# Kernel optimization log

Hardware: AMD Instinct MI355X
Metric: run time of the kernel (lower is better)

Reference implementation:

```python
import jax, jax.numpy as jnp
import numpy as np

N, E, D, H, C = 50000, 800000, 64, 2, 64  # nodes, edges, feat, heads, per-head out


def _transformer_conv(x, src, dst, wq, bq, wk, bk, wv, bv, ws, bs):
    n = x.shape[0]
    q = (x @ wq + bq).reshape(n, H, C)
    k = (x @ wk + bk).reshape(n, H, C)
    v = (x @ wv + bv).reshape(n, H, C)
    qi = q[dst]           # [E,H,C] gather at target nodes
    kj = k[src]           # [E,H,C] gather at source nodes
    vj = v[src]
    alpha = jnp.einsum('ehc,ehc->eh', qi, kj) / jnp.sqrt(jnp.asarray(C, x.dtype))
    # segment softmax over incoming edges of each dst node
    amax = jax.ops.segment_max(alpha, dst, num_segments=n)          # [N,H]
    amax = jnp.where(jnp.isfinite(amax), amax, 0.0)
    ex = jnp.exp(alpha - amax[dst])                                  # [E,H]
    denom = jax.ops.segment_sum(ex, dst, num_segments=n)            # [N,H]
    a = ex / (denom[dst] + 1e-16)
    out = jax.ops.segment_sum(a[:, :, None] * vj, dst, num_segments=n)  # [N,H,C]
    out = out.mean(axis=1)                                           # concat=False -> mean heads
    return out + x @ ws + bs                                         # root (skip) connection


def setup_inputs() -> dict:
    key = jax.random.key(0)
    ks = jax.random.split(key, 20)
    x = jax.random.normal(ks[0], (N, D), dtype=jnp.float32)
    edge_index = jax.random.randint(ks[1], (2, E), 0, N, dtype=jnp.int64)
    s = 1.0 / np.sqrt(D)
    def lin(k, din, dout):
        return jax.random.uniform(k, (din, dout), jnp.float32, -s, s)
    inp = {"x": x, "edge_index": edge_index}
    i = 2
    for l, din in ((1, D), (2, C)):
        for nm, dout in (("wq", H * C), ("wk", H * C), ("wv", H * C), ("ws", C)):
            inp[f"l{l}_{nm}"] = lin(ks[i], din, dout); i += 1
            inp[f"l{l}_{nm.replace('w','b')}"] = jnp.zeros((dout,), jnp.float32)
    return inp


def reference(x, edge_index,
              l1_wq, l1_bq, l1_wk, l1_bk, l1_wv, l1_bv, l1_ws, l1_bs,
              l2_wq, l2_bq, l2_wk, l2_bk, l2_wv, l2_bv, l2_ws, l2_bs):
    src, dst = edge_index[0], edge_index[1]
    h = _transformer_conv(x, src, dst, l1_wq, l1_bq, l1_wk, l1_bk, l1_wv, l1_bv, l1_ws, l1_bs)
    h = _transformer_conv(h, src, dst, l2_wq, l2_bq, l2_wk, l2_bk, l2_wv, l2_bv, l2_ws, l2_bs)
    return h
```

## Files before the change

### kernel.cpp

```cpp
#include <hip/hip_runtime.h>
#include <hip/hip_fp16.h>
#include <math.h>


typedef _Float16 half8 __attribute__((ext_vector_type(8)));
typedef _Float16 half4 __attribute__((ext_vector_type(4)));
typedef float floatx4 __attribute__((ext_vector_type(4)));

struct __align__(16) H8 { __half2 a, b, c, d; };
struct __align__(16) F16x8 { _Float16 v[8]; };

static __device__ inline __half2 shfl_xor_h2(__half2 v, int off) {
    union { __half2 h; int i; } u;
    u.h = v;
    u.i = __shfl_xor(u.i, off);
    return u.h;
}

__global__ __launch_bounds__(256) void prep_w_both(
    const float* __restrict__ W0, const float* __restrict__ B0,
    const float* __restrict__ W1, const float* __restrict__ B1,
    const float* __restrict__ W2, const float* __restrict__ B2,
    const float* __restrict__ W3, const float* __restrict__ B3,
    const float* __restrict__ W4, const float* __restrict__ B4,
    const float* __restrict__ W5, const float* __restrict__ B5,
    const float* __restrict__ W6, const float* __restrict__ B6,
    const float* __restrict__ W7, const float* __restrict__ B7,
    _Float16* __restrict__ wht1, _Float16* __restrict__ wht2,
    float* __restrict__ ball1, float* __restrict__ ball2,
    int* __restrict__ counts, int n) {
    const int tid = blockIdx.x * 256 + threadIdx.x;
    const int nt  = gridDim.x * 256;
    for (int idx = tid; idx < 448 * 64; idx += nt) {
        int c = idx >> 6, k = idx & 63;
        float v1, v2;
        if (c < 128)      { v1 = W0[k*128 + c];       v2 = W4[k*128 + c]; }
        else if (c < 256) { v1 = W1[k*128 + (c-128)]; v2 = W5[k*128 + (c-128)]; }
        else if (c < 384) { v1 = W2[k*128 + (c-256)]; v2 = W6[k*128 + (c-256)]; }
        else              { v1 = W3[k*64 + (c-384)];  v2 = W7[k*64 + (c-384)]; }
        wht1[c*64 + k] = (_Float16)v1;
        wht2[c*64 + k] = (_Float16)v2;
        if (k == 0) {
            float b1, b2;
            if (c < 128)      { b1 = B0[c];     b2 = B4[c]; }
            else if (c < 256) { b1 = B1[c-128]; b2 = B5[c-128]; }
            else if (c < 384) { b1 = B2[c-256]; b2 = B6[c-256]; }
            else              { b1 = B3[c-384]; b2 = B7[c-384]; }
            ball1[c] = b1;
            ball2[c] = b2;
        }
    }
    for (int i = tid; i < n; i += nt) counts[i] = 0;
}

template <int F32IN>
static __device__ __forceinline__ void gemm_tile_body(
    const void* __restrict__ Xin, int rows,
    const _Float16* __restrict__ WhT, const float* __restrict__ Ball,
    _Float16* __restrict__ Qo, _Float16* __restrict__ KVo,
    float* __restrict__ So, int blk, int tix) {
    const int lane = tix & 63;
    const int w    = tix >> 6;
    const int kg   = lane >> 4;
    const int li   = lane & 15;
    const int rbase = blk * 64 + w * 16;
    const int row  = rbase + li;
    const int crow = row < rows ? row : rows - 1;

    half8 a0, a1;
    if constexpr (F32IN) {
        const float* xp = (const float*)Xin + (size_t)crow * 64 + kg * 8;
        float4 f0 = *(const float4*)xp;
        float4 f1 = *(const float4*)(xp + 4);
        float4 f2 = *(const float4*)(xp + 32);
        float4 f3 = *(const float4*)(xp + 36);
        a0 = half8{(_Float16)f0.x, (_Float16)f0.y, (_Float16)f0.z, (_Float16)f0.w,
                   (_Float16)f1.x, (_Float16)f1.y, (_Float16)f1.z, (_Float16)f1.w};
        a1 = half8{(_Float16)f2.x, (_Float16)f2.y, (_Float16)f2.z, (_Float16)f2.w,
                   (_Float16)f3.x, (_Float16)f3.y, (_Float16)f3.z, (_Float16)f3.w};
    } else {
        const _Float16* xp = (const _Float16*)Xin + (size_t)crow * 64 + kg * 8;
        a0 = *(const half8*)xp;
        a1 = *(const half8*)(xp + 32);
    }

#pragma unroll
    for (int tg = 0; tg < 28; tg += 4) {
        half8 b0[4], b1[4];
        float4 bias[4];
#pragma unroll
        for (int j = 0; j < 4; ++j) {
            const _Float16* wp = WhT + (size_t)((tg + j) * 16 + li) * 64 + kg * 8;
            b0[j] = *(const half8*)wp;
            b1[j] = *(const half8*)(wp + 32);
            bias[j] = *(const float4*)(Ball + (tg + j) * 16 + kg * 4);
        }
#pragma unroll
        for (int j = 0; j < 4; ++j) {
            const int t = tg + j;
            floatx4 acc = {0.f, 0.f, 0.f, 0.f};
            acc = __builtin_amdgcn_mfma_f32_16x16x32_f16(b0[j], a0, acc, 0, 0, 0);
            acc = __builtin_amdgcn_mfma_f32_16x16x32_f16(b1[j], a1, acc, 0, 0, 0);
            const int c0 = t * 16 + kg * 4;
            if (row < rows) {
                float o0 = acc[0] + bias[j].x, o1 = acc[1] + bias[j].y;
                float o2 = acc[2] + bias[j].z, o3 = acc[3] + bias[j].w;
                if (t < 8) {
                    *(half4*)(Qo + (size_t)row * 128 + c0) =
                        half4{(_Float16)o0, (_Float16)o1, (_Float16)o2, (_Float16)o3};
                } else if (t < 24) {
                    *(half4*)(KVo + (size_t)row * 256 + (c0 - 128)) =
                        half4{(_Float16)o0, (_Float16)o1, (_Float16)o2, (_Float16)o3};
                } else {
                    *(float4*)(So + (size_t)row * 64 + (c0 - 384)) =
                        make_float4(o0, o1, o2, o3);
                }
            }
        }
    }
}

__global__ __launch_bounds__(256) void gemm1_scatter(
    const float* __restrict__ X, int rows,
    const _Float16* __restrict__ WhT, const float* __restrict__ Ball,
    _Float16* __restrict__ Qo, _Float16* __restrict__ KVo,
    float* __restrict__ So,
    const int* __restrict__ src, const int* __restrict__ dst,
    int* __restrict__ counts, unsigned short* __restrict__ ssrc,
    int e, int gb) {
    const int bid = blockIdx.x;
    const int g = bid / 5;
    if (bid % 5 == 0 && g < gb) {
        gemm_tile_body<1>(X, rows, WhT, Ball, Qo, KVo, So, g, threadIdx.x);
    } else {
        int sblk = bid - g - 1;
        if (bid % 5 == 0) sblk = bid - g;
        int i = sblk * 256 + threadIdx.x;
        if (i < e) {
            int d = dst[i];
            int pos = atomicAdd(&counts[d], 1);
            if (pos < 64) ssrc[((size_t)d << 6) + pos] = (unsigned short)src[i];
        }
    }
}

template <int F32IN>
__global__ __launch_bounds__(256) void gemm_mfma(
    const void* __restrict__ Xin, int rows,
    const _Float16* __restrict__ WhT, const float* __restrict__ Ball,
    _Float16* __restrict__ Qo, _Float16* __restrict__ KVo,
    float* __restrict__ So) {
    gemm_tile_body<F32IN>(Xin, rows, WhT, Ball, Qo, KVo, So,
                          blockIdx.x, threadIdx.x);
}

template <int HALF_OUT>
__global__ __launch_bounds__(256) void attn_kernel(
    const _Float16* __restrict__ Qh,
    const _Float16* __restrict__ KV,
    const int* __restrict__ cnts, const unsigned short* __restrict__ ssrc,
    const float* __restrict__ skip,
    float* __restrict__ outF, _Float16* __restrict__ outH, int n) {
    int node = (blockIdx.x * 256 + threadIdx.x) >> 6;
    int lane = threadIdx.x & 63;
    if (node >= n) return;
    const int slot = lane >> 4;
    const int koff = ((lane >> 3) & 1) * 64 + (lane & 7) * 8;

    H8 q = *(const H8*)(Qh + (size_t)node * 128 + koff);

    const int beg = node << 6;
    int c = cnts[node];
    if (c > 64) c = 64;
    const int end = beg + c;
    float m = -INFINITY, l = 0.f;
    __half2 hz = __float2half2_rn(0.f);
    __half2 ha = hz, hb = hz, hc = hz, hd = hz;

    int i = beg;
    bool b0 = false, b1 = false;
    H8 k0, k1, v0, v1;
    if (i < end) {
        int e0 = i + slot, e1 = i + 4 + slot;
        b0 = e0 < end; b1 = e1 < end;
        int s0 = ssrc[b0 ? e0 : end - 1];
        int s1 = ssrc[b1 ? e1 : end - 1];
        const _Float16* p0 = KV + (size_t)s0 * 256 + koff;
        const _Float16* p1 = KV + (size_t)s1 * 256 + koff;
        k0 = *(const H8*)p0; v0 = *(const H8*)(p0 + 128);
        k1 = *(const H8*)p1; v1 = *(const H8*)(p1 + 128);
    }

    while (i < end) {
        const int inext = i + 8;
        bool nb0 = false, nb1 = false;
        H8 nk0, nk1, nv0, nv1;
        if (inext < end) {
            int e0 = inext + slot, e1 = inext + 4 + slot;
            nb0 = e0 < end; nb1 = e1 < end;
            int s0 = ssrc[nb0 ? e0 : end - 1];
            int s1 = ssrc[nb1 ? e1 : end - 1];
            const _Float16* p0 = KV + (size_t)s0 * 256 + koff;
            const _Float16* p1 = KV + (size_t)s1 * 256 + koff;
            nk0 = *(const H8*)p0; nv0 = *(const H8*)(p0 + 128);
            nk1 = *(const H8*)p1; nv1 = *(const H8*)(p1 + 128);
        }

        __half2 dh0 = __hfma2(q.a, k0.a, __hfma2(q.b, k0.b, __hfma2(q.c, k0.c, __hmul2(q.d, k0.d))));
        __half2 dh1 = __hfma2(q.a, k1.a, __hfma2(q.b, k1.b, __hfma2(q.c, k1.c, __hmul2(q.d, k1.d))));
        __half2 pd = __halves2half2(__hadd(dh0.x, dh0.y), __hadd(dh1.x, dh1.y));
        pd = __hadd2(pd, shfl_xor_h2(pd, 1));
        pd = __hadd2(pd, shfl_xor_h2(pd, 2));
        pd = __hadd2(pd, shfl_xor_h2(pd, 4));
        float d0 = b0 ? __half2float(pd.x) * 0.125f : -INFINITY;
        float d1 = b1 ? __half2float(pd.y) * 0.125f : -INFINITY;

        float mx = fmaxf(fmaxf(d0, d1), m);
        float sc = (m == -INFINITY) ? 0.f : __expf(m - mx);
        float p0e = b0 ? __expf(d0 - mx) : 0.f;
        float p1e = b1 ? __expf(d1 - mx) : 0.f;
        l = fmaf(l, sc, p0e + p1e);

        __half2 hsc = __float2half2_rn(sc);
        __half2 hp0 = __float2half2_rn(p0e);
        __half2 hp1 = __float2half2_rn(p1e);
        ha = __hfma2(hp0, v0.a, __hfma2(hp1, v1.a, __hmul2(ha, hsc)));
        hb = __hfma2(hp0, v0.b, __hfma2(hp1, v1.b, __hmul2(hb, hsc)));
        hc = __hfma2(hp0, v0.c, __hfma2(hp1, v1.c, __hmul2(hc, hsc)));
        hd = __hfma2(hp0, v0.d, __hfma2(hp1, v1.d, __hmul2(hd, hsc)));
        m = mx;

        i = inext;
        b0 = nb0; b1 = nb1;
        k0 = nk0; k1 = nk1; v0 = nv0; v1 = nv1;
    }

    float acc[8];
    {
        float2 t0 = __half22float2(ha), t1 = __half22float2(hb);
        float2 t2 = __half22float2(hc), t3 = __half22float2(hd);
        acc[0] = t0.x; acc[1] = t0.y; acc[2] = t1.x; acc[3] = t1.y;
        acc[4] = t2.x; acc[5] = t2.y; acc[6] = t3.x; acc[7] = t3.y;
    }

#pragma unroll
    for (int off = 16; off <= 32; off <<= 1) {
        float mo = __shfl_xor(m, off);
        float lo = __shfl_xor(l, off);
        float ao[8];
#pragma unroll
        for (int j = 0; j < 8; ++j) ao[j] = __shfl_xor(acc[j], off);
        float mm = fmaxf(m, mo);
        float sa = (m  == -INFINITY) ? 0.f : __expf(m  - mm);
        float sb = (mo == -INFINITY) ? 0.f : __expf(mo - mm);
        l = l * sa + lo * sb;
#pragma unroll
        for (int j = 0; j < 8; ++j) acc[j] = acc[j] * sa + ao[j] * sb;
        m = mm;
    }
    float inv = 1.f / (l + 1e-16f);
    float r[8];
#pragma unroll
    for (int j = 0; j < 8; ++j) r[j] = acc[j] * inv;
#pragma unroll
    for (int j = 0; j < 8; ++j) r[j] = 0.5f * (r[j] + __shfl_xor(r[j], 8));

    if (lane < 8) {
        const float4* sp = (const float4*)(skip + (size_t)node * 64 + lane * 8);
        float4 s0 = sp[0], s1 = sp[1];
        float o[8] = {s0.x + r[0], s0.y + r[1], s0.z + r[2], s0.w + r[3],
                      s1.x + r[4], s1.y + r[5], s1.z + r[6], s1.w + r[7]};
        if (HALF_OUT) {
            F16x8 h;
#pragma unroll
            for (int j = 0; j < 8; ++j) h.v[j] = (_Float16)o[j];
            *(F16x8*)(outH + (size_t)node * 64 + lane * 8) = h;
        } else {
            float4* op = (float4*)(outF + (size_t)node * 64 + lane * 8);
            op[0] = make_float4(o[0], o[1], o[2], o[3]);
            op[1] = make_float4(o[4], o[5], o[6], o[7]);
        }
    }
}

extern "C" void kernel_launch(void* const* d_in, const int* in_sizes, int n_in,
                              void* d_out, int out_size, void* d_ws, size_t ws_size,
                              hipStream_t stream) {
    const float* x  = (const float*)d_in[0];
    const int*   ei = (const int*)d_in[1];
    const int N = in_sizes[0] / 64;
    const int E = in_sizes[1] / 2;

    const float* w[16];
    for (int i = 0; i < 16; ++i) w[i] = (const float*)d_in[2 + i];

    char* base = (char*)d_ws;
    size_t off = 0;
    auto alloc = [&](size_t bytes) {
        void* p = base + off;
        off = (off + bytes + 255) & ~(size_t)255;
        return p;
    };
    _Float16* qh   = (_Float16*)alloc((size_t)N * 128 * 2);
    _Float16* kv   = (_Float16*)alloc((size_t)N * 256 * 2);
    float*    sk1  = (float*)alloc((size_t)N * 64 * 4);
    _Float16* h1h  = (_Float16*)alloc((size_t)N * 64 * 2);
    _Float16* wht1 = (_Float16*)alloc(448 * 64 * 2);
    _Float16* wht2 = (_Float16*)alloc(448 * 64 * 2);
    float*    ball1 = (float*)alloc(448 * 4);
    float*    ball2 = (float*)alloc(448 * 4);
    int* counts    = (int*)alloc((size_t)N * 4);
    unsigned short* ssrc = (unsigned short*)alloc((size_t)N * 64 * 2);

    prep_w_both<<<224, 256, 0, stream>>>(
        w[0], w[1], w[2], w[3], w[4], w[5], w[6], w[7],
        w[8], w[9], w[10], w[11], w[12], w[13], w[14], w[15],
        wht1, wht2, ball1, ball2, counts, N);

    const int eb = (E + 255) / 256;
    const int gb = (N + 63) / 64;
    const int ab = (N * 64 + 255) / 256;

    gemm1_scatter<<<gb + eb, 256, 0, stream>>>(x, N, wht1, ball1, qh, kv, sk1,
                                               ei, ei + E, counts, ssrc, E, gb);

    attn_kernel<1><<<ab, 256, 0, stream>>>(qh, kv, counts, ssrc, sk1,
                                           nullptr, h1h, N);
    gemm_mfma<0><<<gb, 256, 0, stream>>>(h1h, N, wht2, ball2, qh, kv, (float*)d_out);
    attn_kernel<0><<<ab, 256, 0, stream>>>(qh, kv, counts, ssrc, (float*)d_out,
                                           (float*)d_out, nullptr, N);
}
```

Measured before the change: 230.7 us.

## Fuse weight prep with edge scatter and split first GEMM out

Moves the edge bucketing (atomic count plus source slot write) out of the interleaved GEMM+scatter kernel and into the weight-prep kernel. The first projection GEMM becomes its own launch. Counts are now zeroed by a memset instead of inside the prep kernel. This trades overlap of the GEMM with the atomic scatter for simpler, more uniform kernels, and it adds one memset launch.

```diff
diff --git a/kernel.cpp b/kernel.cpp
--- a/kernel.cpp
+++ b/kernel.cpp
@@ -17,7 +17,7 @@
     return u.h;
 }
 
-__global__ __launch_bounds__(256) void prep_w_both(
+__global__ __launch_bounds__(256) void prep_scatter(
     const float* __restrict__ W0, const float* __restrict__ B0,
     const float* __restrict__ W1, const float* __restrict__ B1,
     const float* __restrict__ W2, const float* __restrict__ B2,
@@ -28,42 +28,54 @@
     const float* __restrict__ W7, const float* __restrict__ B7,
     _Float16* __restrict__ wht1, _Float16* __restrict__ wht2,
     float* __restrict__ ball1, float* __restrict__ ball2,
-    int* __restrict__ counts, int n) {
-    const int tid = blockIdx.x * 256 + threadIdx.x;
-    const int nt  = gridDim.x * 256;
-    for (int idx = tid; idx < 448 * 64; idx += nt) {
-        int c = idx >> 6, k = idx & 63;
-        float v1, v2;
-        if (c < 128)      { v1 = W0[k*128 + c];       v2 = W4[k*128 + c]; }
-        else if (c < 256) { v1 = W1[k*128 + (c-128)]; v2 = W5[k*128 + (c-128)]; }
-        else if (c < 384) { v1 = W2[k*128 + (c-256)]; v2 = W6[k*128 + (c-256)]; }
-        else              { v1 = W3[k*64 + (c-384)];  v2 = W7[k*64 + (c-384)]; }
-        wht1[c*64 + k] = (_Float16)v1;
-        wht2[c*64 + k] = (_Float16)v2;
-        if (k == 0) {
-            float b1, b2;
-            if (c < 128)      { b1 = B0[c];     b2 = B4[c]; }
-            else if (c < 256) { b1 = B1[c-128]; b2 = B5[c-128]; }
-            else if (c < 384) { b1 = B2[c-256]; b2 = B6[c-256]; }
-            else              { b1 = B3[c-384]; b2 = B7[c-384]; }
-            ball1[c] = b1;
-            ball2[c] = b2;
-        }
-    }
-    for (int i = tid; i < n; i += nt) counts[i] = 0;
+    const int* __restrict__ src, const int* __restrict__ dst,
+    int* __restrict__ counts, unsigned short* __restrict__ ssrc,
+    int e, int pb) {
+    if ((int)blockIdx.x < pb) {
+        int idx = blockIdx.x * 256 + threadIdx.x;
+        if (idx < 448 * 64) {
+            int c = idx >> 6, k = idx & 63;
+            float v1, v2;
+            if (c < 128)      { v1 = W0[k*128 + c];       v2 = W4[k*128 + c]; }
+            else if (c < 256) { v1 = W1[k*128 + (c-128)]; v2 = W5[k*128 + (c-128)]; }
+            else if (c < 384) { v1 = W2[k*128 + (c-256)]; v2 = W6[k*128 + (c-256)]; }
+            else              { v1 = W3[k*64 + (c-384)];  v2 = W7[k*64 + (c-384)]; }
+            wht1[c*64 + k] = (_Float16)v1;
+            wht2[c*64 + k] = (_Float16)v2;
+            if (k == 0) {
+                float b1, b2;
+                if (c < 128)      { b1 = B0[c];     b2 = B4[c]; }
+                else if (c < 256) { b1 = B1[c-128]; b2 = B5[c-128]; }
+                else if (c < 384) { b1 = B2[c-256]; b2 = B6[c-256]; }
+                else              { b1 = B3[c-384]; b2 = B7[c-384]; }
+                ball1[c] = b1;
+                ball2[c] = b2;
+            }
+        }
+    } else {
+        int i = ((int)blockIdx.x - pb) * 256 + threadIdx.x;
+        if (i < e) {
+            int d = dst[i];
+            int pos = atomicAdd(&counts[d], 1);
+            if (pos < 64) ssrc[((size_t)d << 6) + pos] = (unsigned short)src[i];
+        }
+    }
 }
 
 template <int F32IN>
-static __device__ __forceinline__ void gemm_tile_body(
+__global__ __launch_bounds__(256) void gemm_mfma(
     const void* __restrict__ Xin, int rows,
-    const _Float16* __restrict__ WhT, const float* __restrict__ Ball,
-    _Float16* __restrict__ Qo, _Float16* __restrict__ KVo,
-    float* __restrict__ So, int blk, int tix) {
+    const _Float16* __restrict__ WhT,
+    const float* __restrict__ Ball,
+    _Float16* __restrict__ Qo,
+    _Float16* __restrict__ KVo,
+    float* __restrict__ So) {
+    const int tix  = threadIdx.x;
     const int lane = tix & 63;
     const int w    = tix >> 6;
     const int kg   = lane >> 4;
     const int li   = lane & 15;
-    const int rbase = blk * 64 + w * 16;
+    const int rbase = blockIdx.x * 64 + w * 16;
     const int row  = rbase + li;
     const int crow = row < rows ? row : rows - 1;
 
@@ -120,40 +132,6 @@
     }
 }
 
-__global__ __launch_bounds__(256) void gemm1_scatter(
-    const float* __restrict__ X, int rows,
-    const _Float16* __restrict__ WhT, const float* __restrict__ Ball,
-    _Float16* __restrict__ Qo, _Float16* __restrict__ KVo,
-    float* __restrict__ So,
-    const int* __restrict__ src, const int* __restrict__ dst,
-    int* __restrict__ counts, unsigned short* __restrict__ ssrc,
-    int e, int gb) {
-    const int bid = blockIdx.x;
-    const int g = bid / 5;
-    if (bid % 5 == 0 && g < gb) {
-        gemm_tile_body<1>(X, rows, WhT, Ball, Qo, KVo, So, g, threadIdx.x);
-    } else {
-        int sblk = bid - g - 1;
-        if (bid % 5 == 0) sblk = bid - g;
-        int i = sblk * 256 + threadIdx.x;
-        if (i < e) {
-            int d = dst[i];
-            int pos = atomicAdd(&counts[d], 1);
-            if (pos < 64) ssrc[((size_t)d << 6) + pos] = (unsigned short)src[i];
-        }
-    }
-}
-
-template <int F32IN>
-__global__ __launch_bounds__(256) void gemm_mfma(
-    const void* __restrict__ Xin, int rows,
-    const _Float16* __restrict__ WhT, const float* __restrict__ Ball,
-    _Float16* __restrict__ Qo, _Float16* __restrict__ KVo,
-    float* __restrict__ So) {
-    gemm_tile_body<F32IN>(Xin, rows, WhT, Ball, Qo, KVo, So,
-                          blockIdx.x, threadIdx.x);
-}
-
 template <int HALF_OUT>
 __global__ __launch_bounds__(256) void attn_kernel(
     const _Float16* __restrict__ Qh,
@@ -312,17 +290,20 @@
     int* counts    = (int*)alloc((size_t)N * 4);
     unsigned short* ssrc = (unsigned short*)alloc((size_t)N * 64 * 2);
 
-    prep_w_both<<<224, 256, 0, stream>>>(
+    hipMemsetAsync(counts, 0, (size_t)N * 4, stream);
+
+    const int eb = (E + 255) / 256;
+    const int pb = (448 * 64 + 255) / 256;
+    const int gb = (N + 63) / 64;
+    const int ab = (N * 64 + 255) / 256;
+
+    prep_scatter<<<pb + eb, 256, 0, stream>>>(
         w[0], w[1], w[2], w[3], w[4], w[5], w[6], w[7],
         w[8], w[9], w[10], w[11], w[12], w[13], w[14], w[15],
-        wht1, wht2, ball1, ball2, counts, N);
-
-    const int eb = (E + 255) / 256;
-    const int gb = (N + 63) / 64;
-    const int ab = (N * 64 + 255) / 256;
-
-    gemm1_scatter<<<gb + eb, 256, 0, stream>>>(x, N, wht1, ball1, qh, kv, sk1,
-                                               ei, ei + E, counts, ssrc, E, gb);
+        wht1, wht2, ball1, ball2,
+        ei, ei + E, counts, ssrc, E, pb);
+
+    gemm_mfma<1><<<gb, 256, 0, stream>>>(x, N, wht1, ball1, qh, kv, sk1);
 
     attn_kernel<1><<<ab, 256, 0, stream>>>(qh, kv, counts, ssrc, sk1,
                                            nullptr, h1h, N);
```

After: 247.5 us. +7.3%, slower.
